# Kernel optimization log

Hardware: AMD Instinct MI355X
Metric: run time of the kernel (lower is better)

The kernel has to match this reference:

```python
import jax, jax.numpy as jnp
import numpy as np

B = 16384
NUM_ACTIONS = 308
NUM_STYLES = 4
UNITS = 512
STYLE_UNITS = 32


def _lstm_cell(x, h, c, Wih, Whh, bih, bhh):
    # PyTorch LSTMCell: gates = x @ Wih.T + h @ Whh.T + bih + bhh, order (i, f, g, o)
    g = x @ Wih.T + h @ Whh.T + (bih + bhh)
    i, f, gg, o = jnp.split(g, 4, axis=-1)
    i = jax.nn.sigmoid(i)
    f = jax.nn.sigmoid(f)
    gg = jnp.tanh(gg)
    o = jax.nn.sigmoid(o)
    c2 = f * c + i * gg
    h2 = o * jnp.tanh(c2)
    return h2, c2


def setup_inputs() -> dict:
    key = jax.random.key(0)
    ks = jax.random.split(key, 16)

    def rn(k, shape, fan_in):
        return jax.random.normal(k, shape, dtype=jnp.float32) * (1.0 / np.sqrt(fan_in))

    inp = {
        'x': jax.random.normal(ks[0], (B, NUM_ACTIONS), dtype=jnp.float32),
        'style': jax.random.uniform(ks[1], (B, NUM_STYLES), dtype=jnp.float32),
        'Wsl': rn(ks[2], (STYLE_UNITS, NUM_STYLES), NUM_STYLES),
        'bsl': jnp.zeros((STYLE_UNITS,), jnp.float32),
        'Ws0': rn(ks[3], (NUM_ACTIONS, STYLE_UNITS), STYLE_UNITS),
        'bs0': jnp.zeros((NUM_ACTIONS,), jnp.float32),
        'Ws1': rn(ks[4], (UNITS, STYLE_UNITS), STYLE_UNITS),
        'bs1': jnp.zeros((UNITS,), jnp.float32),
        'Ws2': rn(ks[5], (UNITS, STYLE_UNITS), STYLE_UNITS),
        'bs2': jnp.zeros((UNITS,), jnp.float32),
        'Wih0': rn(ks[6], (4 * UNITS, NUM_ACTIONS), NUM_ACTIONS),
        'Whh0': rn(ks[7], (4 * UNITS, UNITS), UNITS),
        'bih0': jnp.zeros((4 * UNITS,), jnp.float32),
        'bhh0': jnp.zeros((4 * UNITS,), jnp.float32),
        'Wih1': rn(ks[8], (4 * UNITS, UNITS), UNITS),
        'Whh1': rn(ks[9], (4 * UNITS, UNITS), UNITS),
        'bih1': jnp.zeros((4 * UNITS,), jnp.float32),
        'bhh1': jnp.zeros((4 * UNITS,), jnp.float32),
        'Wih2': rn(ks[10], (4 * UNITS, UNITS), UNITS),
        'Whh2': rn(ks[11], (4 * UNITS, UNITS), UNITS),
        'bih2': jnp.zeros((4 * UNITS,), jnp.float32),
        'bhh2': jnp.zeros((4 * UNITS,), jnp.float32),
        'Wout': rn(ks[12], (NUM_ACTIONS, UNITS), UNITS),
        'bout': jnp.zeros((NUM_ACTIONS,), jnp.float32),
    }
    return inp


def reference(x, style, Wsl, bsl, Ws0, bs0, Ws1, bs1, Ws2, bs2,
              Wih0, Whh0, bih0, bhh0, Wih1, Whh1, bih1, bhh1,
              Wih2, Whh2, bih2, bhh2, Wout, bout):
    batch = x.shape[0]
    s = style @ Wsl.T + bsl  # [B, style_units]
    style_params = [(Ws0, bs0), (Ws1, bs1), (Ws2, bs2)]
    lstm_params = [(Wih0, Whh0, bih0, bhh0), (Wih1, Whh1, bih1, bhh1), (Wih2, Whh2, bih2, bhh2)]
    zeros = jnp.zeros((batch, UNITS), dtype=x.dtype)
    states = []
    for l in range(3):
        prev_x = x
        Ws, bs = style_params[l]
        style_act = jnp.tanh(s @ Ws.T + bs)
        x = x + style_act
        Wih, Whh, bih, bhh = lstm_params[l]
        h, c = _lstm_cell(x, zeros, zeros, Wih, Whh, bih, bhh)
        states.append((h, c))
        x = h
        if l != 0:
            x = x + prev_x
    out = x @ Wout.T + bout  # [B, NUM_ACTIONS]
    return (out,) + tuple(t for hc in states for t in hc)
```

## Files before the change

### kernel.cpp

```cpp
#include <hip/hip_runtime.h>
#include <hip/hip_bf16.h>

#define B_SZ 16384
#define NA 308
#define NAP 320
#define UN 512

typedef float f32x4 __attribute__((ext_vector_type(4)));
typedef short bf16x8 __attribute__((ext_vector_type(8)));
typedef unsigned short ushort_t;

constexpr size_t OFF_WB0 = 0;
constexpr size_t OFF_WB1 = 0x100000;
constexpr size_t OFF_WB2 = 0x280000;
constexpr size_t OFF_WOB = 0x400000;
constexpr size_t OFF_B0R = 0x480000;
constexpr size_t OFF_B1R = OFF_B0R + 0x2000;
constexpr size_t OFF_B2R = OFF_B1R + 0x2000;
constexpr size_t OFF_A0  = OFF_B2R + 0x2000;
constexpr size_t OFF_C0  = OFF_A0  + 0x2000;
constexpr size_t OFF_A1  = OFF_C0  + 0x2000;
constexpr size_t OFF_C1  = OFF_A1  + 0x2000;
constexpr size_t OFF_A2  = OFF_C1  + 0x2000;
constexpr size_t OFF_C2  = OFF_A2  + 0x2000;
constexpr size_t OFF_XA  = 0x500000;
constexpr size_t OFF_XB  = OFF_XA + 0x1000000;

__device__ __forceinline__ float sigmoidf_(float x){ return 1.0f/(1.0f+__expf(-x)); }
__device__ __forceinline__ float tanhf_(float x){ return 2.0f/(1.0f+__expf(-2.0f*x)) - 1.0f; }

__device__ __forceinline__ ushort_t f2b(float f){
  union { float f; unsigned int u; } v; v.f = f;
  unsigned int r = v.u + 0x7FFFu + ((v.u >> 16) & 1u);
  return (ushort_t)(r >> 16);
}

__device__ __forceinline__ void gload16(const void* g, void* l){
  __builtin_amdgcn_global_load_lds((__attribute__((address_space(1))) void*)(g),
                                   (__attribute__((address_space(3))) void*)(l), 16, 0, 0);
}

__device__ __forceinline__ int gate_srow(int n){
  int jb = n / 192; int rem = n - jb*192; int t = rem >> 6; int r = rem & 63;
  int g = (t == 0) ? 0 : ((t == 1) ? 1024 : 1536);
  return g + jb*64 + r;
}

__global__ void prep_kernel(
    const float* __restrict__ Wih0, const float* __restrict__ Wih1, const float* __restrict__ Wih2,
    const float* __restrict__ Wout,
    const float* __restrict__ bih0, const float* __restrict__ bhh0,
    const float* __restrict__ bih1, const float* __restrict__ bhh1,
    const float* __restrict__ bih2, const float* __restrict__ bhh2,
    const float* __restrict__ Wsl, const float* __restrict__ bsl,
    const float* __restrict__ Ws0, const float* __restrict__ bs0,
    const float* __restrict__ Ws1, const float* __restrict__ bs1,
    const float* __restrict__ Ws2, const float* __restrict__ bs2,
    char* __restrict__ ws)
{
  const int tid = blockIdx.x*blockDim.x + threadIdx.x;
  const int stride = gridDim.x*blockDim.x;

  const float* WihA[3] = {Wih0, Wih1, Wih2};
  const float* bihA[3] = {bih0, bih1, bih2};
  const float* bhhA[3] = {bhh0, bhh1, bhh2};
  const float* WsA[3]  = {Ws0, Ws1, Ws2};
  const float* bsA[3]  = {bs0, bs1, bs2};
  const int KpA[3] = {NAP, UN, UN};
  const int KrA[3] = {NA, UN, UN};
  const size_t wbOff[3] = {OFF_WB0, OFF_WB1, OFF_WB2};
  const size_t bOff[3]  = {OFF_B0R, OFF_B1R, OFF_B2R};
  const size_t aOff[3]  = {OFF_A0, OFF_A1, OFF_A2};
  const size_t cOff[3]  = {OFF_C0, OFF_C1, OFF_C2};

  #pragma unroll
  for (int ly = 0; ly < 3; ly++){
    ushort_t* dst = (ushort_t*)(ws + wbOff[ly]);
    const float* Wih = WihA[ly];
    const int Kp = KpA[ly], Kr = KrA[ly];
    const int tot = 1536*Kp;
    for (int i = tid; i < tot; i += stride){
      int n = i / Kp, k = i - n*Kp;
      int srow = gate_srow(n);
      float v = (k < Kr) ? Wih[(size_t)srow*Kr + k] : 0.0f;
      dst[i] = f2b(v);
    }
  }
  {
    ushort_t* dst = (ushort_t*)(ws + OFF_WOB);
    for (int i = tid; i < 320*512; i += stride){
      int n = i >> 9, k = i & 511;
      dst[i] = f2b(n < NA ? Wout[(size_t)n*UN + k] : 0.0f);
    }
  }
  #pragma unroll
  for (int ly = 0; ly < 3; ly++){
    float* bd = (float*)(ws + bOff[ly]);
    for (int i = tid; i < 1536; i += stride){
      int srow = gate_srow(i);
      bd[i] = bihA[ly][srow] + bhhA[ly][srow];
    }
  }
  #pragma unroll
  for (int ly = 0; ly < 3; ly++){
    float* Ad = (float*)(ws + aOff[ly]);
    float* cd = (float*)(ws + cOff[ly]);
    const float* Wsp = WsA[ly]; const float* bsp = bsA[ly];
    const int N = (ly == 0) ? NA : UN;
    for (int i = tid; i < N*4; i += stride){
      int n = i >> 2, q = i & 3;
      float s = 0.f;
      #pragma unroll 8
      for (int j = 0; j < 32; j++) s += Wsp[n*32 + j] * Wsl[j*4 + q];
      Ad[i] = s;
    }
    for (int i = tid; i < N; i += stride){
      float s = 0.f;
      #pragma unroll 8
      for (int j = 0; j < 32; j++) s += Wsp[i*32 + j] * bsl[j];
      cd[i] = s + bsp[i];
    }
  }
}

__global__ void b0_kernel(const float* __restrict__ x, const float* __restrict__ style,
                          const float* __restrict__ A0, const float* __restrict__ c0,
                          ushort_t* __restrict__ x0b)
{
  int idx = blockIdx.x*blockDim.x + threadIdx.x;
  const int total = B_SZ * (NAP/8);
  const int stride = gridDim.x*blockDim.x;
  for (int i = idx; i < total; i += stride){
    int b = i / 40;
    int kc = (i - b*40) * 8;
    float4 sty = *(const float4*)(style + b*4);
    unsigned int pk[4];
    #pragma unroll
    for (int h = 0; h < 4; h++){
      ushort_t lo = 0, hi = 0;
      int k0 = kc + h*2;
      if (k0 < NA){
        float4 A = *(const float4*)(A0 + k0*4);
        float tt = sty.x*A.x + sty.y*A.y + sty.z*A.z + sty.w*A.w + c0[k0];
        lo = f2b(x[(size_t)b*NA + k0] + tanhf_(tt));
      }
      if (k0 + 1 < NA){
        float4 A = *(const float4*)(A0 + (k0+1)*4);
        float tt = sty.x*A.x + sty.y*A.y + sty.z*A.z + sty.w*A.w + c0[k0+1];
        hi = f2b(x[(size_t)b*NA + k0 + 1] + tanhf_(tt));
      }
      pk[h] = (unsigned int)lo | ((unsigned int)hi << 16);
    }
    *(uint4*)(x0b + (size_t)i*8) = make_uint4(pk[0], pk[1], pk[2], pk[3]);
  }
}

template<int MODE>
__global__ __launch_bounds__(512, 2)
void gates_kernel(const ushort_t* __restrict__ Xb, int Kpad,
                  const ushort_t* __restrict__ Wb,
                  const float* __restrict__ biasr,
                  float* __restrict__ h_out, float* __restrict__ c_out,
                  const float* __restrict__ style,
                  const float* __restrict__ Anext, const float* __restrict__ cnext,
                  const float* __restrict__ hp0, const float* __restrict__ hp1,
                  ushort_t* __restrict__ xnext)
{
  __shared__ char smem[40960];
  char* ldsX = smem;
  char* ldsW = smem + 16384;

  const int tid = threadIdx.x;
  const int l = tid & 63;
  const int w = tid >> 6;
  const int wm = w >> 1, wn = w & 1;
  const int m0 = blockIdx.x * 128;
  const int jb = blockIdx.y;

  int aoff[2][2], boff[3][2][2];
  #pragma unroll
  for (int mi = 0; mi < 2; mi++){
    int r = wm*32 + mi*16 + (l & 15);
    #pragma unroll
    for (int ks = 0; ks < 2; ks++){
      int c = ks*4 + (l >> 4);
      aoff[mi][ks] = r*128 + ((c ^ (r & 7)) << 4);
    }
  }
  #pragma unroll
  for (int t = 0; t < 3; t++)
    #pragma unroll
    for (int ni = 0; ni < 2; ni++){
      int rr = t*64 + wn*32 + ni*16 + (l & 15);
      #pragma unroll
      for (int ks = 0; ks < 2; ks++){
        int c = ks*4 + (l >> 4);
        boff[t][ni][ks] = rr*128 + ((c ^ (rr & 7)) << 4);
      }
    }

  f32x4 acc[3][2][2] = {};
  const int KT = Kpad >> 6;

  for (int kt = 0; kt < KT; kt++){
    const int k0 = kt << 6;
    #pragma unroll
    for (int it = 0; it < 2; it++){
      int g = it*512 + tid;
      int row = g >> 3, c = g & 7, cs = c ^ (row & 7);
      gload16(Xb + (size_t)(m0 + row)*Kpad + k0 + cs*8, ldsX + g*16);
    }
    #pragma unroll
    for (int it = 0; it < 3; it++){
      int g = it*512 + tid;
      int row = g >> 3, c = g & 7, cs = c ^ (row & 7);
      gload16(Wb + (size_t)(jb*192 + row)*Kpad + k0 + cs*8, ldsW + g*16);
    }
    __syncthreads();

    bf16x8 a[2][2];
    #pragma unroll
    for (int mi = 0; mi < 2; mi++)
      #pragma unroll
      for (int ks = 0; ks < 2; ks++)
        a[mi][ks] = *(const bf16x8*)(ldsX + aoff[mi][ks]);

    #pragma unroll
    for (int t = 0; t < 3; t++){
      bf16x8 bb[2][2];
      #pragma unroll
      for (int ni = 0; ni < 2; ni++)
        #pragma unroll
        for (int ks = 0; ks < 2; ks++)
          bb[ni][ks] = *(const bf16x8*)(ldsW + boff[t][ni][ks]);
      #pragma unroll
      for (int mi = 0; mi < 2; mi++)
        #pragma unroll
        for (int ni = 0; ni < 2; ni++){
          acc[t][mi][ni] = __builtin_amdgcn_mfma_f32_16x16x32_bf16(a[mi][0], bb[ni][0], acc[t][mi][ni], 0, 0, 0);
          acc[t][mi][ni] = __builtin_amdgcn_mfma_f32_16x16x32_bf16(a[mi][1], bb[ni][1], acc[t][mi][ni], 0, 0, 0);
        }
    }
    __syncthreads();
  }

  #pragma unroll
  for (int ni = 0; ni < 2; ni++){
    int jl = wn*32 + ni*16 + (l & 15);
    int j = jb*64 + jl;
    float bi = biasr[jb*192 + jl];
    float bg = biasr[jb*192 + 64 + jl];
    float bo = biasr[jb*192 + 128 + jl];
    float4 An = {0,0,0,0}; float cn = 0.f;
    if constexpr (MODE == 0 || MODE == 1){
      An = *(const float4*)(Anext + j*4);
      cn = cnext[j];
    }
    #pragma unroll
    for (int mi = 0; mi < 2; mi++){
      #pragma unroll
      for (int reg = 0; reg < 4; reg++){
        int m = m0 + wm*32 + mi*16 + ((l >> 4) << 2) + reg;
        float gi = acc[0][mi][ni][reg] + bi;
        float gg = acc[1][mi][ni][reg] + bg;
        float go = acc[2][mi][ni][reg] + bo;
        float iv = sigmoidf_(gi);
        float gv = tanhf_(gg);
        float ov = sigmoidf_(go);
        float cv = iv * gv;
        float hv = ov * tanhf_(cv);
        size_t o = (size_t)m*UN + j;
        c_out[o] = cv;
        h_out[o] = hv;
        float nx = hv;
        if constexpr (MODE == 0){
          float4 sty = *(const float4*)(style + m*4);
          nx += tanhf_(sty.x*An.x + sty.y*An.y + sty.z*An.z + sty.w*An.w + cn);
        } else if constexpr (MODE == 1){
          float4 sty = *(const float4*)(style + m*4);
          nx += hp0[o] + tanhf_(sty.x*An.x + sty.y*An.y + sty.z*An.z + sty.w*An.w + cn);
        } else {
          nx += hp0[o] + hp1[o];
        }
        xnext[o] = f2b(nx);
      }
    }
  }
}

__global__ __launch_bounds__(512, 2)
void out_kernel(const ushort_t* __restrict__ Xb,
                const ushort_t* __restrict__ Wob,
                const float* __restrict__ bout,
                float* __restrict__ out)
{
  __shared__ char smem[24576];
  char* ldsX = smem;
  char* ldsW = smem + 16384;
  const int tid = threadIdx.x;
  const int l = tid & 63;
  const int w = tid >> 6, wm = w >> 1, wn = w & 1;
  const int m0 = blockIdx.x * 128, n0 = blockIdx.y * 64;

  int aoff[2][2], boff[2][2];
  #pragma unroll
  for (int mi = 0; mi < 2; mi++){
    int r = wm*32 + mi*16 + (l & 15);
    #pragma unroll
    for (int ks = 0; ks < 2; ks++){
      int c = ks*4 + (l >> 4);
      aoff[mi][ks] = r*128 + ((c ^ (r & 7)) << 4);
    }
  }
  #pragma unroll
  for (int ni = 0; ni < 2; ni++){
    int rr = wn*32 + ni*16 + (l & 15);
    #pragma unroll
    for (int ks = 0; ks < 2; ks++){
      int c = ks*4 + (l >> 4);
      boff[ni][ks] = rr*128 + ((c ^ (rr & 7)) << 4);
    }
  }

  f32x4 acc[2][2] = {};
  for (int kt = 0; kt < 8; kt++){
    const int k0 = kt << 6;
    #pragma unroll
    for (int it = 0; it < 2; it++){
      int g = it*512 + tid;
      int row = g >> 3, c = g & 7, cs = c ^ (row & 7);
      gload16(Xb + (size_t)(m0 + row)*UN + k0 + cs*8, ldsX + g*16);
    }
    {
      int g = tid;
      int row = g >> 3, c = g & 7, cs = c ^ (row & 7);
      gload16(Wob + (size_t)(n0 + row)*UN + k0 + cs*8, ldsW + g*16);
    }
    __syncthreads();
    bf16x8 a[2][2], b[2][2];
    #pragma unroll
    for (int mi = 0; mi < 2; mi++){
      a[mi][0] = *(const bf16x8*)(ldsX + aoff[mi][0]);
      a[mi][1] = *(const bf16x8*)(ldsX + aoff[mi][1]);
    }
    #pragma unroll
    for (int ni = 0; ni < 2; ni++){
      b[ni][0] = *(const bf16x8*)(ldsW + boff[ni][0]);
      b[ni][1] = *(const bf16x8*)(ldsW + boff[ni][1]);
    }
    #pragma unroll
    for (int mi = 0; mi < 2; mi++)
      #pragma unroll
      for (int ni = 0; ni < 2; ni++){
        acc[mi][ni] = __builtin_amdgcn_mfma_f32_16x16x32_bf16(a[mi][0], b[ni][0], acc[mi][ni], 0, 0, 0);
        acc[mi][ni] = __builtin_amdgcn_mfma_f32_16x16x32_bf16(a[mi][1], b[ni][1], acc[mi][ni], 0, 0, 0);
      }
    __syncthreads();
  }

  #pragma unroll
  for (int ni = 0; ni < 2; ni++){
    int n = n0 + wn*32 + ni*16 + (l & 15);
    if (n < NA){
      float bv = bout[n];
      #pragma unroll
      for (int mi = 0; mi < 2; mi++)
        #pragma unroll
        for (int reg = 0; reg < 4; reg++){
          int m = m0 + wm*32 + mi*16 + ((l >> 4) << 2) + reg;
          out[(size_t)m*NA + n] = acc[mi][ni][reg] + bv;
        }
    }
  }
}

extern "C" void kernel_launch(void* const* d_in, const int* in_sizes, int n_in,
                              void* d_out, int out_size, void* d_ws, size_t ws_size,
                              hipStream_t stream)
{
  const float* x     = (const float*)d_in[0];
  const float* style = (const float*)d_in[1];
  const float* Wsl   = (const float*)d_in[2];
  const float* bsl   = (const float*)d_in[3];
  const float* Ws0   = (const float*)d_in[4];
  const float* bs0   = (const float*)d_in[5];
  const float* Ws1   = (const float*)d_in[6];
  const float* bs1   = (const float*)d_in[7];
  const float* Ws2   = (const float*)d_in[8];
  const float* bs2   = (const float*)d_in[9];
  const float* Wih0  = (const float*)d_in[10];
  const float* bih0  = (const float*)d_in[12];
  const float* bhh0  = (const float*)d_in[13];
  const float* Wih1  = (const float*)d_in[14];
  const float* bih1  = (const float*)d_in[16];
  const float* bhh1  = (const float*)d_in[17];
  const float* Wih2  = (const float*)d_in[18];
  const float* bih2  = (const float*)d_in[20];
  const float* bhh2  = (const float*)d_in[21];
  const float* Wout  = (const float*)d_in[22];
  const float* bout  = (const float*)d_in[23];

  char* ws = (char*)d_ws;
  float* out = (float*)d_out;
  float* h0 = out + (size_t)B_SZ*NA;
  float* c0 = h0 + (size_t)B_SZ*UN;
  float* h1 = c0 + (size_t)B_SZ*UN;
  float* c1 = h1 + (size_t)B_SZ*UN;
  float* h2 = c1 + (size_t)B_SZ*UN;
  float* c2 = h2 + (size_t)B_SZ*UN;

  prep_kernel<<<1024, 256, 0, stream>>>(Wih0, Wih1, Wih2, Wout,
                                        bih0, bhh0, bih1, bhh1, bih2, bhh2,
                                        Wsl, bsl, Ws0, bs0, Ws1, bs1, Ws2, bs2, ws);

  b0_kernel<<<2048, 256, 0, stream>>>(x, style,
                                      (const float*)(ws + OFF_A0), (const float*)(ws + OFF_C0),
                                      (ushort_t*)(ws + OFF_XA));

  gates_kernel<0><<<dim3(128, 8), 512, 0, stream>>>(
      (const ushort_t*)(ws + OFF_XA), NAP,
      (const ushort_t*)(ws + OFF_WB0), (const float*)(ws + OFF_B0R),
      h0, c0, style,
      (const float*)(ws + OFF_A1), (const float*)(ws + OFF_C1),
      nullptr, nullptr, (ushort_t*)(ws + OFF_XB));

  gates_kernel<1><<<dim3(128, 8), 512, 0, stream>>>(
      (const ushort_t*)(ws + OFF_XB), UN,
      (const ushort_t*)(ws + OFF_WB1), (const float*)(ws + OFF_B1R),
      h1, c1, style,
      (const float*)(ws + OFF_A2), (const float*)(ws + OFF_C2),
      h0, nullptr, (ushort_t*)(ws + OFF_XA));

  gates_kernel<2><<<dim3(128, 8), 512, 0, stream>>>(
      (const ushort_t*)(ws + OFF_XA), UN,
      (const ushort_t*)(ws + OFF_WB2), (const float*)(ws + OFF_B2R),
      h2, c2, nullptr, nullptr, nullptr,
      h0, h1, (ushort_t*)(ws + OFF_XB));

  out_kernel<<<dim3(128, 5), 512, 0, stream>>>(
      (const ushort_t*)(ws + OFF_XB), (const ushort_t*)(ws + OFF_WOB), bout, out);

  (void)in_sizes; (void)n_in; (void)out_size; (void)ws_size;
}
```

Measured before the change: 476.7 us.

## Double-buffer LDS K-tiles and stage epilogue through LDS for coalesced stores

Both GEMM kernels now use two LDS buffers so the next K-tile's global loads are issued before the current tile's MFMAs, which removes one barrier per iteration and overlaps load latency with compute. The epilogues write h/c (and out) into padded LDS tiles, then emit row-contiguous float4 stores and vectorized bf16 xnext writes instead of scattered scalar stores. Launch bounds are raised to 4 blocks per CU. LDS per block doubles to 80KB, which may limit occupancy, and the occupancy hint may force register pressure or spills.

New measurement: 444.5 us. 1.07x faster.

```diff
diff --git a/kernel.cpp b/kernel.cpp
--- a/kernel.cpp
+++ b/kernel.cpp
@@ -156,7 +156,7 @@
 }
 
 template<int MODE>
-__global__ __launch_bounds__(512, 2)
+__global__ __launch_bounds__(512, 4)
 void gates_kernel(const ushort_t* __restrict__ Xb, int Kpad,
                   const ushort_t* __restrict__ Wb,
                   const float* __restrict__ biasr,
@@ -166,9 +166,7 @@
                   const float* __restrict__ hp0, const float* __restrict__ hp1,
                   ushort_t* __restrict__ xnext)
 {
-  __shared__ char smem[40960];
-  char* ldsX = smem;
-  char* ldsW = smem + 16384;
+  __shared__ char smem[81920];
 
   const int tid = threadIdx.x;
   const int l = tid & 63;
@@ -202,28 +200,38 @@
   f32x4 acc[3][2][2] = {};
   const int KT = Kpad >> 6;
 
-  for (int kt = 0; kt < KT; kt++){
+  auto stage = [&](int buf, int kt){
+    char* bX = smem + buf*40960;
+    char* bW = bX + 16384;
     const int k0 = kt << 6;
     #pragma unroll
     for (int it = 0; it < 2; it++){
       int g = it*512 + tid;
       int row = g >> 3, c = g & 7, cs = c ^ (row & 7);
-      gload16(Xb + (size_t)(m0 + row)*Kpad + k0 + cs*8, ldsX + g*16);
+      gload16(Xb + (size_t)(m0 + row)*Kpad + k0 + cs*8, bX + g*16);
     }
     #pragma unroll
     for (int it = 0; it < 3; it++){
       int g = it*512 + tid;
       int row = g >> 3, c = g & 7, cs = c ^ (row & 7);
-      gload16(Wb + (size_t)(jb*192 + row)*Kpad + k0 + cs*8, ldsW + g*16);
-    }
-    __syncthreads();
+      gload16(Wb + (size_t)(jb*192 + row)*Kpad + k0 + cs*8, bW + g*16);
+    }
+  };
+
+  stage(0, 0);
+  __syncthreads();
+  int cur = 0;
+  for (int kt = 0; kt < KT; kt++){
+    if (kt + 1 < KT) stage(cur ^ 1, kt + 1);
+    const char* bX = smem + cur*40960;
+    const char* bW = bX + 16384;
 
     bf16x8 a[2][2];
     #pragma unroll
     for (int mi = 0; mi < 2; mi++)
       #pragma unroll
       for (int ks = 0; ks < 2; ks++)
-        a[mi][ks] = *(const bf16x8*)(ldsX + aoff[mi][ks]);
+        a[mi][ks] = *(const bf16x8*)(bX + aoff[mi][ks]);
 
     #pragma unroll
     for (int t = 0; t < 3; t++){
@@ -232,7 +240,7 @@
       for (int ni = 0; ni < 2; ni++)
         #pragma unroll
         for (int ks = 0; ks < 2; ks++)
-          bb[ni][ks] = *(const bf16x8*)(ldsW + boff[t][ni][ks]);
+          bb[ni][ks] = *(const bf16x8*)(bW + boff[t][ni][ks]);
       #pragma unroll
       for (int mi = 0; mi < 2; mi++)
         #pragma unroll
@@ -242,25 +250,23 @@
         }
     }
     __syncthreads();
-  }
+    cur ^= 1;
+  }
+
+  float* lbH = (float*)smem;
+  float* lbC = (float*)(smem + 34816);
 
   #pragma unroll
   for (int ni = 0; ni < 2; ni++){
     int jl = wn*32 + ni*16 + (l & 15);
-    int j = jb*64 + jl;
     float bi = biasr[jb*192 + jl];
     float bg = biasr[jb*192 + 64 + jl];
     float bo = biasr[jb*192 + 128 + jl];
-    float4 An = {0,0,0,0}; float cn = 0.f;
-    if constexpr (MODE == 0 || MODE == 1){
-      An = *(const float4*)(Anext + j*4);
-      cn = cnext[j];
-    }
-    #pragma unroll
-    for (int mi = 0; mi < 2; mi++){
+    #pragma unroll
+    for (int mi = 0; mi < 2; mi++)
       #pragma unroll
       for (int reg = 0; reg < 4; reg++){
-        int m = m0 + wm*32 + mi*16 + ((l >> 4) << 2) + reg;
+        int rl = wm*32 + mi*16 + ((l >> 4) << 2) + reg;
         float gi = acc[0][mi][ni][reg] + bi;
         float gg = acc[1][mi][ni][reg] + bg;
         float go = acc[2][mi][ni][reg] + bo;
@@ -269,34 +275,68 @@
         float ov = sigmoidf_(go);
         float cv = iv * gv;
         float hv = ov * tanhf_(cv);
-        size_t o = (size_t)m*UN + j;
-        c_out[o] = cv;
-        h_out[o] = hv;
-        float nx = hv;
-        if constexpr (MODE == 0){
-          float4 sty = *(const float4*)(style + m*4);
-          nx += tanhf_(sty.x*An.x + sty.y*An.y + sty.z*An.z + sty.w*An.w + cn);
-        } else if constexpr (MODE == 1){
-          float4 sty = *(const float4*)(style + m*4);
-          nx += hp0[o] + tanhf_(sty.x*An.x + sty.y*An.y + sty.z*An.z + sty.w*An.w + cn);
-        } else {
-          nx += hp0[o] + hp1[o];
-        }
-        xnext[o] = f2b(nx);
-      }
-    }
-  }
-}
-
-__global__ __launch_bounds__(512, 2)
+        lbH[rl*68 + jl] = hv;
+        lbC[rl*68 + jl] = cv;
+      }
+  }
+  __syncthreads();
+
+  #pragma unroll
+  for (int q = 0; q < 4; q++){
+    int idx = q*512 + tid;
+    int r = idx >> 4, c4 = idx & 15;
+    size_t go = (size_t)(m0 + r)*UN + jb*64 + c4*4;
+    *(float4*)(h_out + go) = *(const float4*)(lbH + r*68 + c4*4);
+    *(float4*)(c_out + go) = *(const float4*)(lbC + r*68 + c4*4);
+  }
+
+  #pragma unroll
+  for (int q = 0; q < 2; q++){
+    int idx = q*512 + tid;
+    int r = idx >> 3, c8 = idx & 7;
+    int m = m0 + r;
+    const float* hp = lbH + r*68 + c8*8;
+    float hv8[8];
+    *(float4*)(hv8)     = *(const float4*)(hp);
+    *(float4*)(hv8 + 4) = *(const float4*)(hp + 4);
+    float nx[8];
+    if constexpr (MODE == 0 || MODE == 1){
+      float4 sty = *(const float4*)(style + (size_t)m*4);
+      #pragma unroll
+      for (int e = 0; e < 8; e++){
+        int j = jb*64 + c8*8 + e;
+        float4 An = *(const float4*)(Anext + (size_t)j*4);
+        float tt = sty.x*An.x + sty.y*An.y + sty.z*An.z + sty.w*An.w + cnext[j];
+        nx[e] = hv8[e] + tanhf_(tt);
+      }
+      if constexpr (MODE == 1){
+        const float* p = hp0 + (size_t)m*UN + jb*64 + c8*8;
+        float4 p0 = *(const float4*)(p), p1 = *(const float4*)(p + 4);
+        nx[0]+=p0.x; nx[1]+=p0.y; nx[2]+=p0.z; nx[3]+=p0.w;
+        nx[4]+=p1.x; nx[5]+=p1.y; nx[6]+=p1.z; nx[7]+=p1.w;
+      }
+    } else {
+      const float* p = hp0 + (size_t)m*UN + jb*64 + c8*8;
+      const float* s = hp1 + (size_t)m*UN + jb*64 + c8*8;
+      float4 p0 = *(const float4*)(p), p1 = *(const float4*)(p + 4);
+      float4 q0 = *(const float4*)(s), q1 = *(const float4*)(s + 4);
+      nx[0]=hv8[0]+p0.x+q0.x; nx[1]=hv8[1]+p0.y+q0.y; nx[2]=hv8[2]+p0.z+q0.z; nx[3]=hv8[3]+p0.w+q0.w;
+      nx[4]=hv8[4]+p1.x+q1.x; nx[5]=hv8[5]+p1.y+q1.y; nx[6]=hv8[6]+p1.z+q1.z; nx[7]=hv8[7]+p1.w+q1.w;
+    }
+    union { ushort_t u[8]; uint4 v; } pk;
+    #pragma unroll
+    for (int e = 0; e < 8; e++) pk.u[e] = f2b(nx[e]);
+    *(uint4*)(xnext + (size_t)m*UN + jb*64 + c8*8) = pk.v;
+  }
+}
+
+__global__ __launch_bounds__(512, 4)
 void out_kernel(const ushort_t* __restrict__ Xb,
                 const ushort_t* __restrict__ Wob,
                 const float* __restrict__ bout,
                 float* __restrict__ out)
 {
-  __shared__ char smem[24576];
-  char* ldsX = smem;
-  char* ldsW = smem + 16384;
+  __shared__ char smem[49152];
   const int tid = threadIdx.x;
   const int l = tid & 63;
   const int w = tid >> 6, wm = w >> 1, wn = w & 1;
@@ -323,30 +363,41 @@
   }
 
   f32x4 acc[2][2] = {};
-  for (int kt = 0; kt < 8; kt++){
+
+  auto stage = [&](int buf, int kt){
+    char* bX = smem + buf*24576;
+    char* bW = bX + 16384;
     const int k0 = kt << 6;
     #pragma unroll
     for (int it = 0; it < 2; it++){
       int g = it*512 + tid;
       int row = g >> 3, c = g & 7, cs = c ^ (row & 7);
-      gload16(Xb + (size_t)(m0 + row)*UN + k0 + cs*8, ldsX + g*16);
+      gload16(Xb + (size_t)(m0 + row)*UN + k0 + cs*8, bX + g*16);
     }
     {
       int g = tid;
       int row = g >> 3, c = g & 7, cs = c ^ (row & 7);
-      gload16(Wob + (size_t)(n0 + row)*UN + k0 + cs*8, ldsW + g*16);
-    }
-    __syncthreads();
+      gload16(Wob + (size_t)(n0 + row)*UN + k0 + cs*8, bW + g*16);
+    }
+  };
+
+  stage(0, 0);
+  __syncthreads();
+  int cur = 0;
+  for (int kt = 0; kt < 8; kt++){
+    if (kt + 1 < 8) stage(cur ^ 1, kt + 1);
+    const char* bX = smem + cur*24576;
+    const char* bW = bX + 16384;
     bf16x8 a[2][2], b[2][2];
     #pragma unroll
     for (int mi = 0; mi < 2; mi++){
-      a[mi][0] = *(const bf16x8*)(ldsX + aoff[mi][0]);
-      a[mi][1] = *(const bf16x8*)(ldsX + aoff[mi][1]);
+      a[mi][0] = *(const bf16x8*)(bX + aoff[mi][0]);
+      a[mi][1] = *(const bf16x8*)(bX + aoff[mi][1]);
     }
     #pragma unroll
     for (int ni = 0; ni < 2; ni++){
-      b[ni][0] = *(const bf16x8*)(ldsW + boff[ni][0]);
-      b[ni][1] = *(const bf16x8*)(ldsW + boff[ni][1]);
+      b[ni][0] = *(const bf16x8*)(bW + boff[ni][0]);
+      b[ni][1] = *(const bf16x8*)(bW + boff[ni][1]);
     }
     #pragma unroll
     for (int mi = 0; mi < 2; mi++)
@@ -356,21 +407,31 @@
         acc[mi][ni] = __builtin_amdgcn_mfma_f32_16x16x32_bf16(a[mi][1], b[ni][1], acc[mi][ni], 0, 0, 0);
       }
     __syncthreads();
-  }
-
+    cur ^= 1;
+  }
+
+  float* lb = (float*)smem;
   #pragma unroll
   for (int ni = 0; ni < 2; ni++){
-    int n = n0 + wn*32 + ni*16 + (l & 15);
-    if (n < NA){
-      float bv = bout[n];
-      #pragma unroll
-      for (int mi = 0; mi < 2; mi++)
-        #pragma unroll
-        for (int reg = 0; reg < 4; reg++){
-          int m = m0 + wm*32 + mi*16 + ((l >> 4) << 2) + reg;
-          out[(size_t)m*NA + n] = acc[mi][ni][reg] + bv;
-        }
-    }
+    int nl = wn*32 + ni*16 + (l & 15);
+    int n = n0 + nl;
+    float bv = (n < NA) ? bout[n] : 0.0f;
+    #pragma unroll
+    for (int mi = 0; mi < 2; mi++)
+      #pragma unroll
+      for (int reg = 0; reg < 4; reg++){
+        int rl = wm*32 + mi*16 + ((l >> 4) << 2) + reg;
+        lb[rl*68 + nl] = acc[mi][ni][reg] + bv;
+      }
+  }
+  __syncthreads();
+  #pragma unroll
+  for (int q = 0; q < 4; q++){
+    int idx = q*512 + tid;
+    int r = idx >> 4, c4 = idx & 15;
+    int n = n0 + c4*4;
+    if (n <= NA - 4)
+      *(float4*)(out + (size_t)(m0 + r)*NA + n) = *(const float4*)(lb + r*68 + c4*4);
   }
 }
 
```
